# Performance work log

Measured on AMD Instinct MI355X. Metric: run time of the kernel, lower is better.

## Reference

```python
import jax, jax.numpy as jnp
import numpy as np
from math import factorial

# --- constants matching init_kwargs ---
F_MM = 25.0
F_NUMBER = 2.0
PIXEL_SIZE = 3.45e-6  # meters
FOV = 32
N_ZERNIKE = 15
GRID = 256
F_M = F_MM * 1e-3
PUPIL_DIAM = F_M / F_NUMBER
BATCH = 128


def _noll_to_nm(j):
    n = 0
    k = j - 1
    while k > n:
        n += 1
        k -= n
    m = (-1) ** j * ((n % 2) + 2 * ((k + ((n + 1) % 2)) // 2))
    return n, m


def _zernike(n, m, r, theta):
    am = abs(m)
    R = np.zeros_like(r)
    for s in range((n - am) // 2 + 1):
        c = ((-1) ** s * factorial(n - s)
             / (factorial(s) * factorial((n + am) // 2 - s) * factorial((n - am) // 2 - s)))
        R = R + c * r ** (n - 2 * s)
    norm = np.sqrt(n + 1) if m == 0 else np.sqrt(2 * (n + 1))
    ang = np.cos(am * theta) if m >= 0 else np.sin(am * theta)
    return np.where(r <= 1.0, norm * R * ang, 0.0)


def _build_basis(n_modes, gs):
    lin = np.linspace(-1.0, 1.0, gs)
    y, x = np.meshgrid(lin, lin, indexing='ij')
    r = np.sqrt(x ** 2 + y ** 2)
    theta = np.arctan2(y, x)
    basis = np.stack([_zernike(*_noll_to_nm(j), r, theta) for j in range(1, n_modes + 1)]).astype(np.float32)
    aperture = (r <= 1.0).astype(np.float32)
    return basis, aperture


def _grid_sample_bilinear(img, gx, gy):
    # img: [B, G, G]; gx, gy: [H, W] in [-1,1]; align_corners=False, zero padding
    G = img.shape[-1]
    x = ((gx + 1.0) * G - 1.0) * 0.5
    y = ((gy + 1.0) * G - 1.0) * 0.5
    x0 = jnp.floor(x)
    y0 = jnp.floor(y)
    tx = x - x0
    ty = y - y0

    def tap(xf, yf, w):
        valid = (xf >= 0) & (xf <= G - 1) & (yf >= 0) & (yf <= G - 1)
        xi = jnp.clip(xf, 0, G - 1).astype(jnp.int32)
        yi = jnp.clip(yf, 0, G - 1).astype(jnp.int32)
        return img[:, yi, xi] * jnp.where(valid, w, 0.0)[None]

    return (tap(x0, y0, (1.0 - tx) * (1.0 - ty))
            + tap(x0 + 1.0, y0, tx * (1.0 - ty))
            + tap(x0, y0 + 1.0, (1.0 - tx) * ty)
            + tap(x0 + 1.0, y0 + 1.0, tx * ty))


def _compute_psf(coeffs, basis, aperture, wavelengths):
    # coeffs: [B, N]
    opd = jnp.einsum('bn,nij->bij', coeffs, basis)                     # [B,G,G]
    phase = (2.0 * np.pi) * opd[:, None] / wavelengths[None, :, None, None]  # [B,3,G,G]
    pupil = aperture * jnp.exp(1j * phase)                             # complex64
    field = jnp.fft.fftshift(jnp.fft.fft2(jnp.fft.ifftshift(pupil, axes=(-2, -1))), axes=(-2, -1))
    psf_raw = jnp.abs(field) ** 2                                      # [B,3,G,G]
    chans = []
    for i in range(3):
        zoom = PIXEL_SIZE * FOV * PUPIL_DIAM / (wavelengths[i] * F_M * GRID)
        g1 = jnp.arange(FOV, dtype=jnp.float32) / (FOV - 1) * (2.0 * zoom) - zoom  # linspace(-s, s, FOV)
        gy, gx = jnp.meshgrid(g1, g1, indexing='ij')
        chans.append(_grid_sample_bilinear(psf_raw[:, i], gx, gy))     # [B,FOV,FOV]
    psf = jnp.stack(chans, axis=1)                                     # [B,3,FOV,FOV]
    return psf / (psf.sum(axis=(-2, -1), keepdims=True) + 1e-8)


def _defocus_wfe(d_obj, d_focus):
    return F_M ** 2 / (8.0 * F_NUMBER ** 2) * (1.0 / d_focus - 1.0 / (d_obj + 1e-8))


def setup_inputs() -> dict:
    key = jax.random.key(0)
    k1, k2, k3 = jax.random.split(key, 3)
    basis, aperture = _build_basis(N_ZERNIKE, GRID)
    return {
        'd_obj': 1.0 + 4.0 * jax.random.uniform(k1, (BATCH,), dtype=jnp.float32),  # meters in [1,5)
        'current_focus_dist_0': jnp.float32(0.5),
        'current_focus_dist_90': jnp.float32(2.0),
        'zernike_0': 1e-7 * jax.random.normal(k2, (N_ZERNIKE,), dtype=jnp.float32),
        'zernike_90': 1e-7 * jax.random.normal(k3, (N_ZERNIKE,), dtype=jnp.float32),
        'zernike_basis': jnp.asarray(basis),
        'aperture': jnp.asarray(aperture),
        'wavelengths': jnp.asarray(np.array([630e-9, 550e-9, 470e-9], dtype=np.float32)),
    }


def reference(d_obj, current_focus_dist_0, current_focus_dist_90, zernike_0, zernike_90,
              zernike_basis, aperture, wavelengths):
    B = d_obj.shape[0]
    c0 = jnp.tile(zernike_0[None], (B, 1)).at[:, 3].add(_defocus_wfe(d_obj, current_focus_dist_0))
    c90 = jnp.tile(zernike_90[None], (B, 1)).at[:, 3].add(_defocus_wfe(d_obj, current_focus_dist_90))
    psf_0 = _compute_psf(c0, zernike_basis, aperture, wavelengths)
    psf_90 = _compute_psf(c90, zernike_basis, aperture, wavelengths)
    return psf_0, psf_90
```

## Files before the change

kernel.cpp:

```cpp
#include <hip/hip_runtime.h>
#include <hip/hip_bf16.h>

typedef __attribute__((ext_vector_type(8))) short short8;
typedef __attribute__((ext_vector_type(4))) float f32x4;

__device__ __forceinline__ float ldf(const float* p, long long i) { return p[i]; }
__device__ __forceinline__ float ldf(const __hip_bfloat16* p, long long i) { return __bfloat162float(p[i]); }
__device__ __forceinline__ void stf(float* p, long long i, float v) { p[i] = v; }
__device__ __forceinline__ void stf(__hip_bfloat16* p, long long i, float v) { p[i] = __float2bfloat16(v); }

__device__ __forceinline__ unsigned packbf(float a, float b) {
    unsigned ua = __float_as_uint(a), ub = __float_as_uint(b);
    ua += 0x7FFFu + ((ua >> 16) & 1u);
    ub += 0x7FFFu + ((ub >> 16) & 1u);
    return (ua >> 16) | (ub & 0xFFFF0000u);
}
__device__ __forceinline__ unsigned short bf16r(float a) {
    unsigned ua = __float_as_uint(a);
    ua += 0x7FFFu + ((ua >> 16) & 1u);
    return (unsigned short)(ua >> 16);
}
__device__ __forceinline__ unsigned cvtpk(float a, float b) {
    unsigned r;
    asm("v_cvt_pk_bf16_f32 %0, %1, %2" : "=v"(r) : "v"(a), "v"(b));
    return r;
}

union U8 { short8 h; unsigned u[4]; };

__device__ __forceinline__ f32x4 mfma16(short8 a, short8 b, f32x4 c) {
    return __builtin_amdgcn_mfma_f32_16x16x32_bf16(a, b, c, 0, 0, 0);
}

__global__ void optics_probe(const unsigned short* ap16, int* flag) {
    if (threadIdx.x == 0 && blockIdx.x == 0) {
        *flag = (ap16[32896] == 0) ? 0 : 1;
    }
}

template <typename ST, int ID>
__global__ void optics_prep(const ST* z0, const ST* z90, const ST* basis, const ST* ap,
                            const ST* wls, unsigned* ampg, float* z4g,
                            unsigned short* w2g, float* tapsw, const int* flag)
{
    if (*flag != ID) return;
    const int t = threadIdx.x;
    const int blk = blockIdx.x;
    if (blk < 256) {
        __shared__ float zs[30];
        __shared__ float invl[3];
        if (t < 30) zs[t] = (t < 15) ? ldf(z0, t) : ldf(z90, t - 15);
        if (t >= 32 && t < 35) invl[t - 32] = (float)(1.0 / (double)ldf(wls, t - 32));
        __syncthreads();
        const int n = blk, m = t;
        const int px = n * 256 + m;
        float b0 = 0.f, b90 = 0.f, z4v = 0.f;
#pragma unroll
        for (int k = 0; k < 15; ++k) {
            float bv = ldf(basis, (long long)k * 65536 + px);
            b0  = fmaf(zs[k],      bv, b0);
            b90 = fmaf(zs[15 + k], bv, b90);
            if (k == 3) z4v = bv;
        }
        float apv = ldf(ap, px);
        const int idx = ((m >> 3) * 256 + n) * 8 + (m & 7);
        z4g[idx] = z4v;
#pragma unroll
        for (int c = 0; c < 3; ++c) {
#pragma unroll
            for (int pp = 0; pp < 2; ++pp) {
                float rev = (pp ? b90 : b0) * invl[c];
                float sn = __builtin_amdgcn_sinf(rev);
                float cs = __builtin_amdgcn_cosf(rev);
                ampg[(c * 2 + pp) * 65536 + idx] = packbf(apv * cs, apv * sn);
            }
        }
    } else {
        const int c = blk - 256;
        __shared__ int tu[64];
        double lam = (double)ldf(wls, c);
        if (t < 64) {
            double zoom = (3.45e-6 * 32.0 * 0.0125) / (lam * 0.025 * 256.0);
            int s = t >> 1, a = t & 1;
            double g1 = (double)s / 31.0 * (2.0 * zoom) - zoom;
            double x  = ((g1 + 1.0) * 256.0 - 1.0) * 0.5;
            double x0 = floor(x);
            int xi = (int)x0 + a;
            float w = (float)(a ? (x - x0) : (1.0 - (x - x0)));
            tu[t] = xi - 128;
            tapsw[c * 64 + t] = (xi >= 0 && xi <= 255) ? w : 0.f;
        }
        __syncthreads();
        for (int e = 0; e < 128; ++e) {
            int entry = e * 256 + t;
            int s = entry & 15, tap = (entry >> 4) & 63, mo = entry >> 10;
            int m = mo * 8 + (s & 7);
            float rev = (float)(-tu[tap] * (m - 128)) * (1.0f / 256.0f);
            rev -= rintf(rev);
            float v = (s < 8) ? __builtin_amdgcn_cosf(rev) : __builtin_amdgcn_sinf(rev);
            w2g[c * 32768 + entry] = bf16r(v);
        }
    }
}

template <typename ST, int ID>
__global__ void __launch_bounds__(512, 4) optics_main(
    const unsigned* __restrict__ ampg, const float* __restrict__ z4g,
    const unsigned short* __restrict__ w2g, const float* __restrict__ tapsw,
    const ST* __restrict__ dobj, const ST* __restrict__ f0s, const ST* __restrict__ f90s,
    const ST* __restrict__ wls, ST* __restrict__ out, const int* __restrict__ flag)
{
    if (*flag != ID) return;

    __shared__ unsigned short GlR[32 * 264];
    __shared__ unsigned short GlI[32 * 264];
    __shared__ float T[64][65];
    __shared__ float twl[64];
    __shared__ float wred[8];

    const int t = threadIdx.x;
    const int bid = blockIdx.x;
    const int c = bid % 3, b = (bid / 3) & 127, p = bid / 384;
    const int wave = t >> 6, lane = t & 63, li = lane & 15, g = lane >> 4;

    const float lam  = ldf(wls, c);
    const float dfoc = ldf(p ? f90s : f0s, 0);
    const float dob  = ldf(dobj, b);
    const float def  = (float)((0.025 * 0.025 / 32.0) *
                               (1.0 / (double)dfoc - 1.0 / ((double)dob + 1e-8)));
    const float defl = def * (float)(1.0 / (double)lam);

    if (t < 64) twl[t] = tapsw[c * 64 + t];

    const unsigned* ampP = ampg + ((c * 2 + p) << 16);
    const short8* W2v = (const short8*)(w2g + c * 32768);

    f32x4 accR[2][4], accI[2][4];
#pragma unroll
    for (int rt = 0; rt < 2; ++rt)
#pragma unroll
        for (int vt = 0; vt < 4; ++vt) {
            accR[rt][vt] = (f32x4){0.f, 0.f, 0.f, 0.f};
            accI[rt][vt] = (f32x4){0.f, 0.f, 0.f, 0.f};
        }

    const int n0 = wave * 32;
    const int row0 = n0 + li, row1 = n0 + 16 + li;
#pragma unroll 2
    for (int ks = 0; ks < 8; ++ks) {
        const int mo = ks * 4 + g;
        const uint4*  a0p = (const uint4*)(ampP + (mo * 256 + row0) * 8);
        const uint4*  a1p = (const uint4*)(ampP + (mo * 256 + row1) * 8);
        const float4* z0p = (const float4*)(z4g + (mo * 256 + row0) * 8);
        const float4* z1p = (const float4*)(z4g + (mo * 256 + row1) * 8);
        uint4  av[2][2] = {{a0p[0], a0p[1]}, {a1p[0], a1p[1]}};
        float4 zv[2][2] = {{z0p[0], z0p[1]}, {z1p[0], z1p[1]}};

        U8 ar[2], ai[2];
#pragma unroll
        for (int rt = 0; rt < 2; ++rt) {
            float pr[8], pi[8];
#pragma unroll
            for (int jj = 0; jj < 2; ++jj)
#pragma unroll
                for (int e = 0; e < 4; ++e) {
                    const int j = jj * 4 + e;
                    unsigned a = ((const unsigned*)&av[rt][jj])[e];
                    float aRv = __uint_as_float(a << 16);
                    float aIv = __uint_as_float(a & 0xFFFF0000u);
                    float z   = ((const float*)&zv[rt][jj])[e];
                    float rev = defl * z;
                    float sn = __builtin_amdgcn_sinf(rev);
                    float cs = __builtin_amdgcn_cosf(rev);
                    pr[j] = fmaf(-aIv, sn, aRv * cs);
                    pi[j] = fmaf( aRv, sn, aIv * cs);
                }
#pragma unroll
            for (int q2 = 0; q2 < 4; ++q2) {
                ar[rt].u[q2] = cvtpk(pr[2 * q2], pr[2 * q2 + 1]);
                ai[rt].u[q2] = cvtpk(pi[2 * q2], pi[2 * q2 + 1]);
            }
        }
#pragma unroll
        for (int vt = 0; vt < 4; ++vt) {
            const short8* wp = W2v + ((mo * 64 + vt * 16 + li) << 1);
            U8 bR, bI, bN;
            bR.h = wp[0];
            bI.h = wp[1];
#pragma unroll
            for (int q2 = 0; q2 < 4; ++q2) bN.u[q2] = bI.u[q2] ^ 0x80008000u;
#pragma unroll
            for (int rt = 0; rt < 2; ++rt) {
                accR[rt][vt] = mfma16(ar[rt].h, bR.h, accR[rt][vt]);
                accR[rt][vt] = mfma16(ai[rt].h, bN.h, accR[rt][vt]);
                accI[rt][vt] = mfma16(ar[rt].h, bI.h, accI[rt][vt]);
                accI[rt][vt] = mfma16(ai[rt].h, bR.h, accI[rt][vt]);
            }
        }
    }

    const int ut = wave >> 1, vt2 = wave & 1;
#pragma unroll
    for (int h = 0; h < 2; ++h) {
        if (h) __syncthreads();
#pragma unroll
        for (int rt = 0; rt < 2; ++rt)
#pragma unroll
            for (int v2 = 0; v2 < 2; ++v2) {
                const f32x4 r4 = accR[rt][2 * h + v2];
                const f32x4 i4 = accI[rt][2 * h + v2];
                const int off = (v2 * 16 + li) * 528 + (n0 + rt * 16 + g * 4) * 2;
                *(uint2*)((char*)GlR + off) = make_uint2(cvtpk(r4[0], r4[1]), cvtpk(r4[2], r4[3]));
                *(uint2*)((char*)GlI + off) = make_uint2(cvtpk(i4[0], i4[1]), cvtpk(i4[2], i4[3]));
            }
        __syncthreads();

        f32x4 fR = {0.f, 0.f, 0.f, 0.f}, fI = {0.f, 0.f, 0.f, 0.f};
        const int urow = ut * 16 + li;
        const int voff0 = (vt2 * 16 + li) * 528;
#pragma unroll 2
        for (int ksb = 0; ksb < 8; ++ksb) {
            const int no = ksb * 4 + g;
            const short8* wp = W2v + ((no * 64 + urow) << 1);
            U8 aWr, aWi, aWn;
            aWr.h = wp[0];
            aWi.h = wp[1];
#pragma unroll
            for (int q2 = 0; q2 < 4; ++q2) aWn.u[q2] = aWi.u[q2] ^ 0x80008000u;
            const int off = voff0 + no * 16;
            short8 gr = *(const short8*)((const char*)GlR + off);
            short8 gi = *(const short8*)((const char*)GlI + off);
            fR = mfma16(aWr.h, gr, fR);
            fR = mfma16(aWn.h, gi, fR);
            fI = mfma16(aWr.h, gi, fI);
            fI = mfma16(aWi.h, gr, fI);
        }
#pragma unroll
        for (int r = 0; r < 4; ++r)
            T[ut * 16 + g * 4 + r][h * 32 + vt2 * 16 + li] = fmaf(fR[r], fR[r], fI[r] * fI[r]);
    }
    __syncthreads();

    float vals[2]; float part = 0.f;
#pragma unroll
    for (int k = 0; k < 2; ++k) {
        int o = t + (k << 9);
        int oy = o >> 5, ox = o & 31;
        float wy0 = twl[2 * oy], wy1 = twl[2 * oy + 1];
        float wx0 = twl[2 * ox], wx1 = twl[2 * ox + 1];
        float acc = wy0 * (wx0 * T[2 * oy][2 * ox]     + wx1 * T[2 * oy][2 * ox + 1])
                  + wy1 * (wx0 * T[2 * oy + 1][2 * ox] + wx1 * T[2 * oy + 1][2 * ox + 1]);
        vals[k] = acc; part += acc;
    }
    for (int off = 32; off; off >>= 1) part += __shfl_down(part, off, 64);
    if (lane == 0) wred[wave] = part;
    __syncthreads();
    float S = 0.f;
#pragma unroll
    for (int wv = 0; wv < 8; ++wv) S += wred[wv];
    float inv = 1.f / (S + 1e-8f);
    long long obase = (long long)p * 393216 + (long long)b * 3072 + (long long)c * 1024;
    stf(out, obase + t,       vals[0] * inv);
    stf(out, obase + t + 512, vals[1] * inv);
}

extern "C" void kernel_launch(void* const* d_in, const int* in_sizes, int n_in,
                              void* d_out, int out_size, void* d_ws, size_t ws_size,
                              hipStream_t stream)
{
    unsigned* ampg = (unsigned*)d_ws;
    float* z4g = (float*)((char*)d_ws + 1572864);
    unsigned short* w2g = (unsigned short*)((char*)d_ws + 1835008);
    float* tapsw = (float*)((char*)d_ws + 2031616);
    int* flag = (int*)((char*)d_ws + 2032384);

    optics_probe<<<1, 64, 0, stream>>>((const unsigned short*)d_in[6], flag);

    optics_prep<__hip_bfloat16, 1><<<259, 256, 0, stream>>>(
        (const __hip_bfloat16*)d_in[3], (const __hip_bfloat16*)d_in[4],
        (const __hip_bfloat16*)d_in[5], (const __hip_bfloat16*)d_in[6],
        (const __hip_bfloat16*)d_in[7], ampg, z4g, w2g, tapsw, flag);
    optics_prep<float, 0><<<259, 256, 0, stream>>>(
        (const float*)d_in[3], (const float*)d_in[4],
        (const float*)d_in[5], (const float*)d_in[6],
        (const float*)d_in[7], ampg, z4g, w2g, tapsw, flag);

    optics_main<__hip_bfloat16, 1><<<768, 512, 0, stream>>>(
        ampg, z4g, w2g, tapsw,
        (const __hip_bfloat16*)d_in[0], (const __hip_bfloat16*)d_in[1],
        (const __hip_bfloat16*)d_in[2], (const __hip_bfloat16*)d_in[7],
        (__hip_bfloat16*)d_out, flag);
    optics_main<float, 0><<<768, 512, 0, stream>>>(
        ampg, z4g, w2g, tapsw,
        (const float*)d_in[0], (const float*)d_in[1],
        (const float*)d_in[2], (const float*)d_in[7],
        (float*)d_out, flag);
}
```

Before: 65.07 us.

## Exploit radial symmetry of defocus term, merge dtype dispatch kernels, alias LDS

The main kernel now pairs each pupil element with its point-reflected partner (row 255-n, column 31-mo reversed). The defocus z4 value is symmetric under that reflection, so each sin/cos pair and each z4 load serves two amplitude samples, halving transcendental work and z4 traffic. The separate probe kernel and the duplicate per-dtype launches are replaced by one prep and one main kernel that check the dtype in-kernel, cutting launch count from five to two. The T buffer now aliases the Gl shared buffers, and launch bounds drop from 4 to 3 waves/blocks per CU, which trades occupancy for registers.

```diff
diff --git a/kernel.cpp b/kernel.cpp
--- a/kernel.cpp
+++ b/kernel.cpp
@@ -32,18 +32,15 @@
     return __builtin_amdgcn_mfma_f32_16x16x32_bf16(a, b, c, 0, 0, 0);
 }
 
-__global__ void optics_probe(const unsigned short* ap16, int* flag) {
-    if (threadIdx.x == 0 && blockIdx.x == 0) {
-        *flag = (ap16[32896] == 0) ? 0 : 1;
-    }
-}
-
-template <typename ST, int ID>
-__global__ void optics_prep(const ST* z0, const ST* z90, const ST* basis, const ST* ap,
-                            const ST* wls, unsigned* ampg, float* z4g,
-                            unsigned short* w2g, float* tapsw, const int* flag)
-{
-    if (*flag != ID) return;
+__device__ __forceinline__ bool is_bf16(const void* apraw) {
+    return ((const unsigned short*)apraw)[32896] != 0;
+}
+
+template <typename ST>
+__device__ __forceinline__ void prep_impl(const ST* z0, const ST* z90, const ST* basis,
+        const ST* ap, const ST* wls, unsigned* ampg, float* z4g,
+        unsigned short* w2g, float* tapsw)
+{
     const int t = threadIdx.x;
     const int blk = blockIdx.x;
     if (blk < 256) {
@@ -103,20 +100,29 @@
     }
 }
 
-template <typename ST, int ID>
-__global__ void __launch_bounds__(512, 4) optics_main(
+__global__ void optics_prep(const void* z0, const void* z90, const void* basis,
+        const void* ap, const void* wls, unsigned* ampg, float* z4g,
+        unsigned short* w2g, float* tapsw)
+{
+    if (is_bf16(ap))
+        prep_impl<__hip_bfloat16>((const __hip_bfloat16*)z0, (const __hip_bfloat16*)z90,
+            (const __hip_bfloat16*)basis, (const __hip_bfloat16*)ap,
+            (const __hip_bfloat16*)wls, ampg, z4g, w2g, tapsw);
+    else
+        prep_impl<float>((const float*)z0, (const float*)z90, (const float*)basis,
+            (const float*)ap, (const float*)wls, ampg, z4g, w2g, tapsw);
+}
+
+template <typename ST>
+__device__ __forceinline__ void main_impl(
     const unsigned* __restrict__ ampg, const float* __restrict__ z4g,
     const unsigned short* __restrict__ w2g, const float* __restrict__ tapsw,
-    const ST* __restrict__ dobj, const ST* __restrict__ f0s, const ST* __restrict__ f90s,
-    const ST* __restrict__ wls, ST* __restrict__ out, const int* __restrict__ flag)
-{
-    if (*flag != ID) return;
-
-    __shared__ unsigned short GlR[32 * 264];
-    __shared__ unsigned short GlI[32 * 264];
-    __shared__ float T[64][65];
+    const ST* dobj, const ST* f0s, const ST* f90s, const ST* wls, ST* out)
+{
+    __shared__ unsigned short Gl[2][32 * 264];
     __shared__ float twl[64];
     __shared__ float wred[8];
+    float* T = (float*)&Gl[0][0];
 
     const int t = threadIdx.x;
     const int bid = blockIdx.x;
@@ -144,75 +150,113 @@
             accI[rt][vt] = (f32x4){0.f, 0.f, 0.f, 0.f};
         }
 
-    const int n0 = wave * 32;
-    const int row0 = n0 + li, row1 = n0 + 16 + li;
-#pragma unroll 2
-    for (int ks = 0; ks < 8; ++ks) {
-        const int mo = ks * 4 + g;
-        const uint4*  a0p = (const uint4*)(ampP + (mo * 256 + row0) * 8);
-        const uint4*  a1p = (const uint4*)(ampP + (mo * 256 + row1) * 8);
-        const float4* z0p = (const float4*)(z4g + (mo * 256 + row0) * 8);
-        const float4* z1p = (const float4*)(z4g + (mo * 256 + row1) * 8);
-        uint4  av[2][2] = {{a0p[0], a0p[1]}, {a1p[0], a1p[1]}};
-        float4 zv[2][2] = {{z0p[0], z0p[1]}, {z1p[0], z1p[1]}};
-
-        U8 ar[2], ai[2];
-#pragma unroll
-        for (int rt = 0; rt < 2; ++rt) {
-            float pr[8], pi[8];
-#pragma unroll
-            for (int jj = 0; jj < 2; ++jj)
-#pragma unroll
-                for (int e = 0; e < 4; ++e) {
-                    const int j = jj * 4 + e;
-                    unsigned a = ((const unsigned*)&av[rt][jj])[e];
-                    float aRv = __uint_as_float(a << 16);
-                    float aIv = __uint_as_float(a & 0xFFFF0000u);
-                    float z   = ((const float*)&zv[rt][jj])[e];
-                    float rev = defl * z;
-                    float sn = __builtin_amdgcn_sinf(rev);
-                    float cs = __builtin_amdgcn_cosf(rev);
-                    pr[j] = fmaf(-aIv, sn, aRv * cs);
-                    pi[j] = fmaf( aRv, sn, aIv * cs);
+    const int n0 = wave * 16;
+    const int nm = 255 - n0;
+    const int rA = n0 + li;
+    const int rB = nm - li;
+
+#pragma unroll 1
+    for (int ks = 0; ks < 4; ++ks) {
+        const int mo = ks * 4 + g, mop = 31 - mo;
+        const float4* zp = (const float4*)(z4g + (mo * 256 + rA) * 8);
+        float4 zlo = zp[0], zhi = zp[1];
+        const uint4* a0p = (const uint4*)(ampP + (mo  * 256 + rA) * 8);
+        const uint4* a1p = (const uint4*)(ampP + (mo  * 256 + rB) * 8);
+        const uint4* a2p = (const uint4*)(ampP + (mop * 256 + rA) * 8);
+        const uint4* a3p = (const uint4*)(ampP + (mop * 256 + rB) * 8);
+        uint4 aw0[2] = {a0p[0], a0p[1]}, aw1[2] = {a1p[0], a1p[1]};
+        uint4 aw2[2] = {a2p[0], a2p[1]}, aw3[2] = {a3p[0], a3p[1]};
+
+        float cs8[8], sn8[8];
+#pragma unroll
+        for (int e = 0; e < 4; ++e) {
+            float r0 = defl * ((const float*)&zlo)[e];
+            sn8[e]     = __builtin_amdgcn_sinf(r0);
+            cs8[e]     = __builtin_amdgcn_cosf(r0);
+            float r1 = defl * ((const float*)&zhi)[e];
+            sn8[4 + e] = __builtin_amdgcn_sinf(r1);
+            cs8[4 + e] = __builtin_amdgcn_cosf(r1);
+        }
+
+        auto mk = [&](const uint4* aw, bool rv, U8& fr, U8& fi) {
+#pragma unroll
+            for (int q = 0; q < 4; ++q) {
+                float pr2[2], pi2[2];
+#pragma unroll
+                for (int s = 0; s < 2; ++s) {
+                    const int e = 2 * q + s;
+                    unsigned a = ((const unsigned*)aw)[e];
+                    float aR = __uint_as_float(a << 16);
+                    float aI = __uint_as_float(a & 0xFFFF0000u);
+                    const int rj = rv ? 7 - e : e;
+                    pr2[s] = fmaf(-aI, sn8[rj], aR * cs8[rj]);
+                    pi2[s] = fmaf( aR, sn8[rj], aI * cs8[rj]);
                 }
-#pragma unroll
-            for (int q2 = 0; q2 < 4; ++q2) {
-                ar[rt].u[q2] = cvtpk(pr[2 * q2], pr[2 * q2 + 1]);
-                ai[rt].u[q2] = cvtpk(pi[2 * q2], pi[2 * q2 + 1]);
+                fr.u[q] = cvtpk(pr2[0], pr2[1]);
+                fi.u[q] = cvtpk(pi2[0], pi2[1]);
             }
-        }
+        };
+
+        U8 f0r, f0i, f1r, f1i;
+        mk(aw0, false, f0r, f0i);
+        mk(aw1, false, f1r, f1i);
 #pragma unroll
         for (int vt = 0; vt < 4; ++vt) {
             const short8* wp = W2v + ((mo * 64 + vt * 16 + li) << 1);
             U8 bR, bI, bN;
-            bR.h = wp[0];
-            bI.h = wp[1];
-#pragma unroll
-            for (int q2 = 0; q2 < 4; ++q2) bN.u[q2] = bI.u[q2] ^ 0x80008000u;
-#pragma unroll
-            for (int rt = 0; rt < 2; ++rt) {
-                accR[rt][vt] = mfma16(ar[rt].h, bR.h, accR[rt][vt]);
-                accR[rt][vt] = mfma16(ai[rt].h, bN.h, accR[rt][vt]);
-                accI[rt][vt] = mfma16(ar[rt].h, bI.h, accI[rt][vt]);
-                accI[rt][vt] = mfma16(ai[rt].h, bR.h, accI[rt][vt]);
-            }
+            bR.h = wp[0]; bI.h = wp[1];
+#pragma unroll
+            for (int q = 0; q < 4; ++q) bN.u[q] = bI.u[q] ^ 0x80008000u;
+            accR[0][vt] = mfma16(f0r.h, bR.h, accR[0][vt]);
+            accR[0][vt] = mfma16(f0i.h, bN.h, accR[0][vt]);
+            accI[0][vt] = mfma16(f0r.h, bI.h, accI[0][vt]);
+            accI[0][vt] = mfma16(f0i.h, bR.h, accI[0][vt]);
+            accR[1][vt] = mfma16(f1r.h, bR.h, accR[1][vt]);
+            accR[1][vt] = mfma16(f1i.h, bN.h, accR[1][vt]);
+            accI[1][vt] = mfma16(f1r.h, bI.h, accI[1][vt]);
+            accI[1][vt] = mfma16(f1i.h, bR.h, accI[1][vt]);
+        }
+        mk(aw2, true, f0r, f0i);
+        mk(aw3, true, f1r, f1i);
+#pragma unroll
+        for (int vt = 0; vt < 4; ++vt) {
+            const short8* wp = W2v + ((mop * 64 + vt * 16 + li) << 1);
+            U8 bR, bI, bN;
+            bR.h = wp[0]; bI.h = wp[1];
+#pragma unroll
+            for (int q = 0; q < 4; ++q) bN.u[q] = bI.u[q] ^ 0x80008000u;
+            accR[0][vt] = mfma16(f0r.h, bR.h, accR[0][vt]);
+            accR[0][vt] = mfma16(f0i.h, bN.h, accR[0][vt]);
+            accI[0][vt] = mfma16(f0r.h, bI.h, accI[0][vt]);
+            accI[0][vt] = mfma16(f0i.h, bR.h, accI[0][vt]);
+            accR[1][vt] = mfma16(f1r.h, bR.h, accR[1][vt]);
+            accR[1][vt] = mfma16(f1i.h, bN.h, accR[1][vt]);
+            accI[1][vt] = mfma16(f1r.h, bI.h, accI[1][vt]);
+            accI[1][vt] = mfma16(f1i.h, bR.h, accI[1][vt]);
         }
     }
 
     const int ut = wave >> 1, vt2 = wave & 1;
+    f32x4 p4[2];
 #pragma unroll
     for (int h = 0; h < 2; ++h) {
         if (h) __syncthreads();
 #pragma unroll
-        for (int rt = 0; rt < 2; ++rt)
-#pragma unroll
-            for (int v2 = 0; v2 < 2; ++v2) {
-                const f32x4 r4 = accR[rt][2 * h + v2];
-                const f32x4 i4 = accI[rt][2 * h + v2];
-                const int off = (v2 * 16 + li) * 528 + (n0 + rt * 16 + g * 4) * 2;
-                *(uint2*)((char*)GlR + off) = make_uint2(cvtpk(r4[0], r4[1]), cvtpk(r4[2], r4[3]));
-                *(uint2*)((char*)GlI + off) = make_uint2(cvtpk(i4[0], i4[1]), cvtpk(i4[2], i4[3]));
+        for (int v2 = 0; v2 < 2; ++v2) {
+            const int vt = 2 * h + v2;
+            {
+                const f32x4 a = accR[0][vt], bb = accI[0][vt];
+                const int off = (v2 * 16 + li) * 528 + (n0 + g * 4) * 2;
+                *(uint2*)((char*)&Gl[0][0] + off) = make_uint2(cvtpk(a[0], a[1]),  cvtpk(a[2], a[3]));
+                *(uint2*)((char*)&Gl[1][0] + off) = make_uint2(cvtpk(bb[0], bb[1]), cvtpk(bb[2], bb[3]));
             }
+            {
+                const f32x4 a = accR[1][vt], bb = accI[1][vt];
+                const int off = (v2 * 16 + li) * 528 + (nm - g * 4 - 3) * 2;
+                *(uint2*)((char*)&Gl[0][0] + off) = make_uint2(cvtpk(a[3], a[2]),  cvtpk(a[1], a[0]));
+                *(uint2*)((char*)&Gl[1][0] + off) = make_uint2(cvtpk(bb[3], bb[2]), cvtpk(bb[1], bb[0]));
+            }
+        }
         __syncthreads();
 
         f32x4 fR = {0.f, 0.f, 0.f, 0.f}, fI = {0.f, 0.f, 0.f, 0.f};
@@ -223,22 +267,25 @@
             const int no = ksb * 4 + g;
             const short8* wp = W2v + ((no * 64 + urow) << 1);
             U8 aWr, aWi, aWn;
-            aWr.h = wp[0];
-            aWi.h = wp[1];
-#pragma unroll
-            for (int q2 = 0; q2 < 4; ++q2) aWn.u[q2] = aWi.u[q2] ^ 0x80008000u;
+            aWr.h = wp[0]; aWi.h = wp[1];
+#pragma unroll
+            for (int q = 0; q < 4; ++q) aWn.u[q] = aWi.u[q] ^ 0x80008000u;
             const int off = voff0 + no * 16;
-            short8 gr = *(const short8*)((const char*)GlR + off);
-            short8 gi = *(const short8*)((const char*)GlI + off);
+            short8 gr = *(const short8*)((const char*)&Gl[0][0] + off);
+            short8 gi = *(const short8*)((const char*)&Gl[1][0] + off);
             fR = mfma16(aWr.h, gr, fR);
             fR = mfma16(aWn.h, gi, fR);
             fI = mfma16(aWr.h, gi, fI);
             fI = mfma16(aWi.h, gr, fI);
         }
+        p4[h] = fR * fR + fI * fI;
+    }
+    __syncthreads();
+#pragma unroll
+    for (int h = 0; h < 2; ++h)
 #pragma unroll
         for (int r = 0; r < 4; ++r)
-            T[ut * 16 + g * 4 + r][h * 32 + vt2 * 16 + li] = fmaf(fR[r], fR[r], fI[r] * fI[r]);
-    }
+            T[(ut * 16 + g * 4 + r) * 65 + h * 32 + vt2 * 16 + li] = p4[h][r];
     __syncthreads();
 
     float vals[2]; float part = 0.f;
@@ -248,8 +295,8 @@
         int oy = o >> 5, ox = o & 31;
         float wy0 = twl[2 * oy], wy1 = twl[2 * oy + 1];
         float wx0 = twl[2 * ox], wx1 = twl[2 * ox + 1];
-        float acc = wy0 * (wx0 * T[2 * oy][2 * ox]     + wx1 * T[2 * oy][2 * ox + 1])
-                  + wy1 * (wx0 * T[2 * oy + 1][2 * ox] + wx1 * T[2 * oy + 1][2 * ox + 1]);
+        float acc = wy0 * (wx0 * T[(2 * oy) * 65 + 2 * ox]     + wx1 * T[(2 * oy) * 65 + 2 * ox + 1])
+                  + wy1 * (wx0 * T[(2 * oy + 1) * 65 + 2 * ox] + wx1 * T[(2 * oy + 1) * 65 + 2 * ox + 1]);
         vals[k] = acc; part += acc;
     }
     for (int off = 32; off; off >>= 1) part += __shfl_down(part, off, 64);
@@ -264,6 +311,23 @@
     stf(out, obase + t + 512, vals[1] * inv);
 }
 
+__global__ void __launch_bounds__(512, 3) optics_main(
+    const unsigned* __restrict__ ampg, const float* __restrict__ z4g,
+    const unsigned short* __restrict__ w2g, const float* __restrict__ tapsw,
+    const void* dobj, const void* f0s, const void* f90s, const void* apraw,
+    const void* wls, void* out)
+{
+    if (is_bf16(apraw))
+        main_impl<__hip_bfloat16>(ampg, z4g, w2g, tapsw,
+            (const __hip_bfloat16*)dobj, (const __hip_bfloat16*)f0s,
+            (const __hip_bfloat16*)f90s, (const __hip_bfloat16*)wls,
+            (__hip_bfloat16*)out);
+    else
+        main_impl<float>(ampg, z4g, w2g, tapsw,
+            (const float*)dobj, (const float*)f0s, (const float*)f90s,
+            (const float*)wls, (float*)out);
+}
+
 extern "C" void kernel_launch(void* const* d_in, const int* in_sizes, int n_in,
                               void* d_out, int out_size, void* d_ws, size_t ws_size,
                               hipStream_t stream)
@@ -272,27 +336,10 @@
     float* z4g = (float*)((char*)d_ws + 1572864);
     unsigned short* w2g = (unsigned short*)((char*)d_ws + 1835008);
     float* tapsw = (float*)((char*)d_ws + 2031616);
-    int* flag = (int*)((char*)d_ws + 2032384);
-
-    optics_probe<<<1, 64, 0, stream>>>((const unsigned short*)d_in[6], flag);
-
-    optics_prep<__hip_bfloat16, 1><<<259, 256, 0, stream>>>(
-        (const __hip_bfloat16*)d_in[3], (const __hip_bfloat16*)d_in[4],
-        (const __hip_bfloat16*)d_in[5], (const __hip_bfloat16*)d_in[6],
-        (const __hip_bfloat16*)d_in[7], ampg, z4g, w2g, tapsw, flag);
-    optics_prep<float, 0><<<259, 256, 0, stream>>>(
-        (const float*)d_in[3], (const float*)d_in[4],
-        (const float*)d_in[5], (const float*)d_in[6],
-        (const float*)d_in[7], ampg, z4g, w2g, tapsw, flag);
-
-    optics_main<__hip_bfloat16, 1><<<768, 512, 0, stream>>>(
-        ampg, z4g, w2g, tapsw,
-        (const __hip_bfloat16*)d_in[0], (const __hip_bfloat16*)d_in[1],
-        (const __hip_bfloat16*)d_in[2], (const __hip_bfloat16*)d_in[7],
-        (__hip_bfloat16*)d_out, flag);
-    optics_main<float, 0><<<768, 512, 0, stream>>>(
-        ampg, z4g, w2g, tapsw,
-        (const float*)d_in[0], (const float*)d_in[1],
-        (const float*)d_in[2], (const float*)d_in[7],
-        (float*)d_out, flag);
-}
+
+    optics_prep<<<259, 256, 0, stream>>>(d_in[3], d_in[4], d_in[5], d_in[6], d_in[7],
+                                         ampg, z4g, w2g, tapsw);
+    optics_main<<<768, 512, 0, stream>>>(ampg, z4g, w2g, tapsw,
+                                         d_in[0], d_in[1], d_in[2], d_in[6], d_in[7],
+                                         d_out);
+}
```

After: 59.24 us. 1.1x faster.

## Use 1024-thread blocks with full-tile LDS staging for the second DFT pass

Applied to the files above, without the earlier changes.

The main kernel now runs with 16 waves per block, each owning 16 rows of the first complex DFT stage instead of 32. The whole 64x256 intermediate goes into LDS in one pass, replacing the two-half loop with its extra barriers, and each thread then produces one output pixel. This aims to raise parallelism per block and cut the serialized half-iterations. It also doubles LDS usage and thread count per block, which may limit occupancy. The prep kernel additionally range-reduces the pupil phase before sin/cos, which mainly affects accuracy.

```diff
diff --git a/kernel.cpp b/kernel.cpp
--- a/kernel.cpp
+++ b/kernel.cpp
@@ -70,6 +70,7 @@
 #pragma unroll
             for (int pp = 0; pp < 2; ++pp) {
                 float rev = (pp ? b90 : b0) * invl[c];
+                rev -= rintf(rev);
                 float sn = __builtin_amdgcn_sinf(rev);
                 float cs = __builtin_amdgcn_cosf(rev);
                 ampg[(c * 2 + pp) * 65536 + idx] = packbf(apv * cs, apv * sn);
@@ -93,8 +94,8 @@
         __syncthreads();
         for (int e = 0; e < 128; ++e) {
             int entry = e * 256 + t;
-            int s = entry & 15, tap = (entry >> 4) & 63, mo = entry >> 10;
-            int m = mo * 8 + (s & 7);
+            int s = entry & 15, tap = (entry >> 4) & 63, oct = entry >> 10;
+            int m = oct * 8 + (s & 7);
             float rev = (float)(-tu[tap] * (m - 128)) * (1.0f / 256.0f);
             rev -= rintf(rev);
             float v = (s < 8) ? __builtin_amdgcn_cosf(rev) : __builtin_amdgcn_sinf(rev);
@@ -104,7 +105,7 @@
 }
 
 template <typename ST, int ID>
-__global__ void __launch_bounds__(512, 4) optics_main(
+__global__ void __launch_bounds__(1024, 4) optics_main(
     const unsigned* __restrict__ ampg, const float* __restrict__ z4g,
     const unsigned short* __restrict__ w2g, const float* __restrict__ tapsw,
     const ST* __restrict__ dobj, const ST* __restrict__ f0s, const ST* __restrict__ f90s,
@@ -112,11 +113,10 @@
 {
     if (*flag != ID) return;
 
-    __shared__ unsigned short GlR[32 * 264];
-    __shared__ unsigned short GlI[32 * 264];
-    __shared__ float T[64][65];
+    __shared__ unsigned short GtR[64 * 264];
+    __shared__ unsigned short GtI[64 * 264];
     __shared__ float twl[64];
-    __shared__ float wred[8];
+    __shared__ float wred[16];
 
     const int t = threadIdx.x;
     const int bid = blockIdx.x;
@@ -135,40 +135,35 @@
     const unsigned* ampP = ampg + ((c * 2 + p) << 16);
     const short8* W2v = (const short8*)(w2g + c * 32768);
 
-    f32x4 accR[2][4], accI[2][4];
-#pragma unroll
-    for (int rt = 0; rt < 2; ++rt)
-#pragma unroll
-        for (int vt = 0; vt < 4; ++vt) {
-            accR[rt][vt] = (f32x4){0.f, 0.f, 0.f, 0.f};
-            accI[rt][vt] = (f32x4){0.f, 0.f, 0.f, 0.f};
-        }
-
-    const int n0 = wave * 32;
-    const int row0 = n0 + li, row1 = n0 + 16 + li;
+    f32x4 gaR[4], gaI[4];
+#pragma unroll
+    for (int vt = 0; vt < 4; ++vt) {
+        gaR[vt] = (f32x4){0.f, 0.f, 0.f, 0.f};
+        gaI[vt] = (f32x4){0.f, 0.f, 0.f, 0.f};
+    }
+
+    const int n0 = wave * 16;
+    const int row = n0 + li;
 #pragma unroll 2
     for (int ks = 0; ks < 8; ++ks) {
-        const int mo = ks * 4 + g;
-        const uint4*  a0p = (const uint4*)(ampP + (mo * 256 + row0) * 8);
-        const uint4*  a1p = (const uint4*)(ampP + (mo * 256 + row1) * 8);
-        const float4* z0p = (const float4*)(z4g + (mo * 256 + row0) * 8);
-        const float4* z1p = (const float4*)(z4g + (mo * 256 + row1) * 8);
-        uint4  av[2][2] = {{a0p[0], a0p[1]}, {a1p[0], a1p[1]}};
-        float4 zv[2][2] = {{z0p[0], z0p[1]}, {z1p[0], z1p[1]}};
-
-        U8 ar[2], ai[2];
-#pragma unroll
-        for (int rt = 0; rt < 2; ++rt) {
+        const int oct = ks * 4 + g;
+        const uint4*  ap4 = (const uint4*)(ampP + (oct * 256 + row) * 8);
+        const float4* zp  = (const float4*)(z4g + (oct * 256 + row) * 8);
+        uint4  av[2] = {ap4[0], ap4[1]};
+        float4 zv[2] = {zp[0], zp[1]};
+
+        U8 ar, ai;
+        {
             float pr[8], pi[8];
 #pragma unroll
             for (int jj = 0; jj < 2; ++jj)
 #pragma unroll
                 for (int e = 0; e < 4; ++e) {
                     const int j = jj * 4 + e;
-                    unsigned a = ((const unsigned*)&av[rt][jj])[e];
+                    unsigned a = ((const unsigned*)&av[jj])[e];
                     float aRv = __uint_as_float(a << 16);
                     float aIv = __uint_as_float(a & 0xFFFF0000u);
-                    float z   = ((const float*)&zv[rt][jj])[e];
+                    float z   = ((const float*)&zv[jj])[e];
                     float rev = defl * z;
                     float sn = __builtin_amdgcn_sinf(rev);
                     float cs = __builtin_amdgcn_cosf(rev);
@@ -177,91 +172,76 @@
                 }
 #pragma unroll
             for (int q2 = 0; q2 < 4; ++q2) {
-                ar[rt].u[q2] = cvtpk(pr[2 * q2], pr[2 * q2 + 1]);
-                ai[rt].u[q2] = cvtpk(pi[2 * q2], pi[2 * q2 + 1]);
+                ar.u[q2] = cvtpk(pr[2 * q2], pr[2 * q2 + 1]);
+                ai.u[q2] = cvtpk(pi[2 * q2], pi[2 * q2 + 1]);
             }
         }
 #pragma unroll
         for (int vt = 0; vt < 4; ++vt) {
-            const short8* wp = W2v + ((mo * 64 + vt * 16 + li) << 1);
+            const short8* wp = W2v + ((oct * 64 + vt * 16 + li) << 1);
             U8 bR, bI, bN;
             bR.h = wp[0];
             bI.h = wp[1];
 #pragma unroll
             for (int q2 = 0; q2 < 4; ++q2) bN.u[q2] = bI.u[q2] ^ 0x80008000u;
-#pragma unroll
-            for (int rt = 0; rt < 2; ++rt) {
-                accR[rt][vt] = mfma16(ar[rt].h, bR.h, accR[rt][vt]);
-                accR[rt][vt] = mfma16(ai[rt].h, bN.h, accR[rt][vt]);
-                accI[rt][vt] = mfma16(ar[rt].h, bI.h, accI[rt][vt]);
-                accI[rt][vt] = mfma16(ai[rt].h, bR.h, accI[rt][vt]);
-            }
-        }
-    }
-
-    const int ut = wave >> 1, vt2 = wave & 1;
-#pragma unroll
-    for (int h = 0; h < 2; ++h) {
-        if (h) __syncthreads();
-#pragma unroll
-        for (int rt = 0; rt < 2; ++rt)
-#pragma unroll
-            for (int v2 = 0; v2 < 2; ++v2) {
-                const f32x4 r4 = accR[rt][2 * h + v2];
-                const f32x4 i4 = accI[rt][2 * h + v2];
-                const int off = (v2 * 16 + li) * 528 + (n0 + rt * 16 + g * 4) * 2;
-                *(uint2*)((char*)GlR + off) = make_uint2(cvtpk(r4[0], r4[1]), cvtpk(r4[2], r4[3]));
-                *(uint2*)((char*)GlI + off) = make_uint2(cvtpk(i4[0], i4[1]), cvtpk(i4[2], i4[3]));
-            }
-        __syncthreads();
-
-        f32x4 fR = {0.f, 0.f, 0.f, 0.f}, fI = {0.f, 0.f, 0.f, 0.f};
-        const int urow = ut * 16 + li;
-        const int voff0 = (vt2 * 16 + li) * 528;
+            gaR[vt] = mfma16(ar.h, bR.h, gaR[vt]);
+            gaR[vt] = mfma16(ai.h, bN.h, gaR[vt]);
+            gaI[vt] = mfma16(ar.h, bI.h, gaI[vt]);
+            gaI[vt] = mfma16(ai.h, bR.h, gaI[vt]);
+        }
+    }
+
+#pragma unroll
+    for (int vt = 0; vt < 4; ++vt) {
+        const int off = (vt * 16 + li) * 264 + n0 + g * 4;
+        *(uint2*)&GtR[off] = make_uint2(cvtpk(gaR[vt][0], gaR[vt][1]), cvtpk(gaR[vt][2], gaR[vt][3]));
+        *(uint2*)&GtI[off] = make_uint2(cvtpk(gaI[vt][0], gaI[vt][1]), cvtpk(gaI[vt][2], gaI[vt][3]));
+    }
+    __syncthreads();
+
+    const int ut = wave >> 2, vt2 = wave & 3;
+    const int urow = ut * 16 + li;
+    const int vrow = (vt2 * 16 + li) * 264;
+    f32x4 fR = {0.f, 0.f, 0.f, 0.f}, fI = {0.f, 0.f, 0.f, 0.f};
 #pragma unroll 2
-        for (int ksb = 0; ksb < 8; ++ksb) {
-            const int no = ksb * 4 + g;
-            const short8* wp = W2v + ((no * 64 + urow) << 1);
-            U8 aWr, aWi, aWn;
-            aWr.h = wp[0];
-            aWi.h = wp[1];
-#pragma unroll
-            for (int q2 = 0; q2 < 4; ++q2) aWn.u[q2] = aWi.u[q2] ^ 0x80008000u;
-            const int off = voff0 + no * 16;
-            short8 gr = *(const short8*)((const char*)GlR + off);
-            short8 gi = *(const short8*)((const char*)GlI + off);
-            fR = mfma16(aWr.h, gr, fR);
-            fR = mfma16(aWn.h, gi, fR);
-            fI = mfma16(aWr.h, gi, fI);
-            fI = mfma16(aWi.h, gr, fI);
-        }
-#pragma unroll
-        for (int r = 0; r < 4; ++r)
-            T[ut * 16 + g * 4 + r][h * 32 + vt2 * 16 + li] = fmaf(fR[r], fR[r], fI[r] * fI[r]);
-    }
-    __syncthreads();
-
-    float vals[2]; float part = 0.f;
-#pragma unroll
-    for (int k = 0; k < 2; ++k) {
-        int o = t + (k << 9);
-        int oy = o >> 5, ox = o & 31;
-        float wy0 = twl[2 * oy], wy1 = twl[2 * oy + 1];
-        float wx0 = twl[2 * ox], wx1 = twl[2 * ox + 1];
-        float acc = wy0 * (wx0 * T[2 * oy][2 * ox]     + wx1 * T[2 * oy][2 * ox + 1])
-                  + wy1 * (wx0 * T[2 * oy + 1][2 * ox] + wx1 * T[2 * oy + 1][2 * ox + 1]);
-        vals[k] = acc; part += acc;
-    }
+    for (int ksb = 0; ksb < 8; ++ksb) {
+        const int no = ksb * 4 + g;
+        const short8* wp = W2v + ((no * 64 + urow) << 1);
+        U8 aWr, aWi, aWn;
+        aWr.h = wp[0];
+        aWi.h = wp[1];
+#pragma unroll
+        for (int q2 = 0; q2 < 4; ++q2) aWn.u[q2] = aWi.u[q2] ^ 0x80008000u;
+        const short8 gr = *(const short8*)&GtR[vrow + no * 8];
+        const short8 gi = *(const short8*)&GtI[vrow + no * 8];
+        fR = mfma16(aWr.h, gr, fR);
+        fR = mfma16(aWn.h, gi, fR);
+        fI = mfma16(aWr.h, gi, fI);
+        fI = mfma16(aWi.h, gr, fI);
+    }
+    f32x4 p4 = fR * fR + fI * fI;
+    __syncthreads();
+    float* T = (float*)GtR;
+#pragma unroll
+    for (int r = 0; r < 4; ++r)
+        T[(ut * 16 + g * 4 + r) * 65 + vt2 * 16 + li] = p4[r];
+    __syncthreads();
+
+    const int oy = t >> 5, ox = t & 31;
+    const float wy0 = twl[2 * oy], wy1 = twl[2 * oy + 1];
+    const float wx0 = twl[2 * ox], wx1 = twl[2 * ox + 1];
+    const float acc = wy0 * (wx0 * T[(2 * oy) * 65 + 2 * ox]     + wx1 * T[(2 * oy) * 65 + 2 * ox + 1])
+                    + wy1 * (wx0 * T[(2 * oy + 1) * 65 + 2 * ox] + wx1 * T[(2 * oy + 1) * 65 + 2 * ox + 1]);
+    float part = acc;
     for (int off = 32; off; off >>= 1) part += __shfl_down(part, off, 64);
     if (lane == 0) wred[wave] = part;
     __syncthreads();
     float S = 0.f;
 #pragma unroll
-    for (int wv = 0; wv < 8; ++wv) S += wred[wv];
-    float inv = 1.f / (S + 1e-8f);
-    long long obase = (long long)p * 393216 + (long long)b * 3072 + (long long)c * 1024;
-    stf(out, obase + t,       vals[0] * inv);
-    stf(out, obase + t + 512, vals[1] * inv);
+    for (int wv = 0; wv < 16; ++wv) S += wred[wv];
+    const float inv = 1.f / (S + 1e-8f);
+    const long long obase = (long long)p * 393216 + (long long)b * 3072 + (long long)c * 1024;
+    stf(out, obase + t, acc * inv);
 }
 
 extern "C" void kernel_launch(void* const* d_in, const int* in_sizes, int n_in,
@@ -285,12 +265,12 @@
         (const float*)d_in[5], (const float*)d_in[6],
         (const float*)d_in[7], ampg, z4g, w2g, tapsw, flag);
 
-    optics_main<__hip_bfloat16, 1><<<768, 512, 0, stream>>>(
+    optics_main<__hip_bfloat16, 1><<<768, 1024, 0, stream>>>(
         ampg, z4g, w2g, tapsw,
         (const __hip_bfloat16*)d_in[0], (const __hip_bfloat16*)d_in[1],
         (const __hip_bfloat16*)d_in[2], (const __hip_bfloat16*)d_in[7],
         (__hip_bfloat16*)d_out, flag);
-    optics_main<float, 0><<<768, 512, 0, stream>>>(
+    optics_main<float, 0><<<768, 1024, 0, stream>>>(
         ampg, z4g, w2g, tapsw,
         (const float*)d_in[0], (const float*)d_in[1],
         (const float*)d_in[2], (const float*)d_in[7],
```

New measurement: 72.52 us. 1.11x slower.
